# Kernel tuning notes

Hardware: AMD Instinct MI355X
Metric: run time of the kernel (lower is better)

The kernel has to match this reference:

```python
import jax, jax.numpy as jnp
import numpy as np

D_MODEL = 1024
NUM_HEADS = 16
D_K = D_MODEL // NUM_HEADS


def setup_inputs() -> dict:
    key = jax.random.key(0)
    ks = jax.random.split(key, 9)
    s = 1.0 / np.sqrt(D_MODEL)
    inp = {
        "x": jax.random.normal(ks[0], (4, 2048, D_MODEL), dtype=jnp.float32),
        "W_q": jax.random.uniform(ks[1], (D_MODEL, D_MODEL), jnp.float32, -s, s),
        "b_q": jax.random.uniform(ks[2], (D_MODEL,), jnp.float32, -s, s),
        "W_k": jax.random.uniform(ks[3], (D_MODEL, D_MODEL), jnp.float32, -s, s),
        "b_k": jax.random.uniform(ks[4], (D_MODEL,), jnp.float32, -s, s),
        "W_v": jax.random.uniform(ks[5], (D_MODEL, D_MODEL), jnp.float32, -s, s),
        "b_v": jax.random.uniform(ks[6], (D_MODEL,), jnp.float32, -s, s),
        "W_o": jax.random.uniform(ks[7], (D_MODEL, D_MODEL), jnp.float32, -s, s),
        "b_o": jax.random.uniform(ks[8], (D_MODEL,), jnp.float32, -s, s),
    }
    return inp


def reference(x, W_q, b_q, W_k, b_k, W_v, b_v, W_o, b_o):
    B, S, _ = x.shape
    # Linear layers (torch convention: y = x @ W.T + b), split into heads -> [B, H, S, d_k]
    def proj(W, b):
        y = jnp.einsum("bsd,ed->bse", x, W) + b
        return y.reshape(B, S, NUM_HEADS, D_K).transpose(0, 2, 1, 3)

    Q = proj(W_q, b_q)
    K = proj(W_k, b_k)
    V = proj(W_v, b_v)

    scale = 1.0 / jnp.sqrt(jnp.asarray(D_K, dtype=x.dtype))
    scores = jnp.einsum("bhqd,bhkd->bhqk", Q, K) * scale  # [B, H, S, S]
    attn = jax.nn.softmax(scores, axis=-1)
    out = jnp.einsum("bhqk,bhkd->bhqd", attn, V)  # [B, H, S, d_k]
    out = out.transpose(0, 2, 1, 3).reshape(B, S, D_MODEL)
    return jnp.einsum("bsd,ed->bse", out, W_o) + b_o
```

## Files before the change

### kernel.cpp

```cpp
#include <hip/hip_runtime.h>
#include <hip/hip_bf16.h>
#include <math.h>


constexpr int D = 1024;
constexpr int H = 16;
constexpr int DK = 64;
constexpr int PSTR = 72;

typedef unsigned short u16;
typedef __attribute__((ext_vector_type(8))) short v8s;
typedef __attribute__((ext_vector_type(4))) float v4f;
typedef const __attribute__((address_space(1))) void gvoid;
typedef __attribute__((address_space(3))) void lvoid;
typedef __attribute__((address_space(3))) u16 ls_u16;
typedef __attribute__((address_space(3))) v8s lv8s;

__device__ __forceinline__ u16 rne_bf16(float f) {
  unsigned u = __float_as_uint(f);
  u += 0x7FFFu + ((u >> 16) & 1u);
  return (u16)(u >> 16);
}

__device__ __forceinline__ unsigned pk_bf16(float a, float b) {
  __hip_bfloat162 t = __float22bfloat162_rn(float2{a, b});
  return *reinterpret_cast<unsigned*>(&t);
}

__device__ __forceinline__ void cfence() { asm volatile("" ::: "memory"); }

__device__ __forceinline__ void split_body(const float* __restrict__ in,
                                           u16* __restrict__ hi, u16* __restrict__ lo,
                                           int i)
{
  const float4 v = ((const float4*)in)[i];
  const float f[4] = {v.x, v.y, v.z, v.w};
  ushort4 h, l;
  u16 hh[4], ll[4];
#pragma unroll
  for (int j = 0; j < 4; ++j) {
    const unsigned u = __float_as_uint(f[j]);
    hh[j] = (u16)(u >> 16);
    const float hf = __uint_as_float(u & 0xFFFF0000u);
    ll[j] = rne_bf16(f[j] - hf);
  }
  h.x = hh[0]; h.y = hh[1]; h.z = hh[2]; h.w = hh[3];
  l.x = ll[0]; l.y = ll[1]; l.z = ll[2]; l.w = ll[3];
  ((ushort4*)hi)[i] = h;
  ((ushort4*)lo)[i] = l;
}

__global__ __launch_bounds__(256) void split_all_kernel(
    const float* __restrict__ x,
    const float* __restrict__ w0, const float* __restrict__ w1,
    const float* __restrict__ w2, const float* __restrict__ w3,
    u16* __restrict__ xs_hi, u16* __restrict__ xs_lo,
    u16* __restrict__ qkv_hi, u16* __restrict__ qkv_lo,
    u16* __restrict__ o_hi, u16* __restrict__ o_lo, int n4x)
{
  constexpr int N4W = (int)(D * (size_t)D / 4);
  const int i = blockIdx.x * 256 + threadIdx.x;
  if (i < n4x) {
    split_body(x, xs_hi, xs_lo, i);
    return;
  }
  const int t = i - n4x;
  const int y = t / N4W;
  const int j = t - y * N4W;
  if (y >= 4) return;
  const float* src = (y == 0) ? w0 : (y == 1) ? w1 : (y == 2) ? w2 : w3;
  const size_t off = (size_t)y * (size_t)(D * (size_t)D);
  u16* hi = (y < 3) ? qkv_hi + off : o_hi;
  u16* lo = (y < 3) ? qkv_lo + off : o_lo;
  split_body(src, hi, lo, j);
}

template<int R>
__device__ __forceinline__ void stage_arr(const u16* __restrict__ src, ls_u16* dst,
                                          int tid, int row0, int k0)
{
  const int cg = (tid & 3) ^ ((tid >> 3) & 3);
#pragma unroll
  for (int j = 0; j < R / 128; ++j) {
    const int row = j * 128 + (tid >> 2);
    __builtin_amdgcn_global_load_lds(
        (gvoid*)(src + (size_t)(row0 + row) * D + k0 + cg * 8),
        (lvoid*)(dst + j * 4096 + tid * 8), 16, 0, 0);
  }
}

template<int EPI>
__global__ __launch_bounds__(512, 2) void gemm_pipe_kernel(
    const u16* __restrict__ Ahi, const u16* __restrict__ Alo,
    const u16* __restrict__ Whi, const u16* __restrict__ Wlo,
    const float* __restrict__ b0v, const float* __restrict__ b1v, const float* __restrict__ b2v,
    u16* __restrict__ Qb, u16* __restrict__ Kb, u16* __restrict__ Vtb,
    float* __restrict__ C, int S_)
{
  constexpr int BM = 256, BN = 256;
  constexpr int TA = BM * 32;
  constexpr int TB = BN * 32;
  constexpr int BUFSZ = 2 * TA + 2 * TB;
  __shared__ u16 lds[2][BUFSZ];

  const int tid = threadIdx.x;
  const int lane = tid & 63, w = tid >> 6;
  const int wm = (w >> 2) * 128, wn = (w & 3) * 64;
  const int fr = lane & 15, fq = lane >> 4;
  const int csw = (fq ^ ((fr >> 1) & 3)) * 8;

  const int gx = gridDim.x;
  const int gyd = gridDim.y;
  const int nwg = gx * gyd;
  int id = blockIdx.y * gx + blockIdx.x;
  id = (id & 7) * (nwg >> 3) + (id >> 3);
  constexpr int GM = 4;
  const int per_grp = GM * gyd;
  const int grp = id / per_grp;
  const int ing = id - grp * per_grp;
  const int m0 = (grp * GM + (ing & (GM - 1))) * BM;
  const int n0 = (ing / GM) * BN;

  v4f acc[8][4];
#pragma unroll
  for (int mi = 0; mi < 8; ++mi)
#pragma unroll
    for (int ni = 0; ni < 4; ++ni) acc[mi][ni] = (v4f){0.f, 0.f, 0.f, 0.f};

  ls_u16* pb0 = (ls_u16*)&lds[0][0];
  ls_u16* pb1 = (ls_u16*)&lds[1][0];

  int aoff[8], boff[4];
#pragma unroll
  for (int i = 0; i < 8; ++i) aoff[i] = (wm + i * 16 + fr) * 32 + csw;
#pragma unroll
  for (int i = 0; i < 4; ++i) boff[i] = 2 * TA + (wn + i * 16 + fr) * 32 + csw;

  stage_arr<BM>(Ahi, pb0, tid, m0, 0);
  stage_arr<BM>(Alo, pb0 + TA, tid, m0, 0);
  stage_arr<BN>(Whi, pb0 + 2 * TA, tid, n0, 0);
  stage_arr<BN>(Wlo, pb0 + 2 * TA + TB, tid, n0, 0);
  asm volatile("s_waitcnt vmcnt(0)" ::: "memory");
  __builtin_amdgcn_s_barrier();
  cfence();

#pragma unroll 2
  for (int k = 0; k < 32; ++k) {
    const int ks = (k + 1 < 32) ? (k + 1) * 32 : 31 * 32;

    v8s ah[8], bh[4], tf[8];
#pragma unroll
    for (int i = 0; i < 8; ++i) ah[i] = *(const lv8s*)(pb0 + aoff[i]);
#pragma unroll
    for (int i = 0; i < 4; ++i) bh[i] = *(const lv8s*)(pb0 + boff[i]);
    stage_arr<BM>(Ahi, pb1, tid, m0, ks);
    stage_arr<BM>(Alo, pb1 + TA, tid, m0, ks);
    __builtin_amdgcn_s_setprio(1);
#pragma unroll
    for (int mi = 0; mi < 8; ++mi)
#pragma unroll
      for (int ni = 0; ni < 4; ++ni)
        acc[mi][ni] = __builtin_amdgcn_mfma_f32_16x16x32_bf16(ah[mi], bh[ni], acc[mi][ni], 0, 0, 0);
    __builtin_amdgcn_s_setprio(0);
    cfence();
    __builtin_amdgcn_s_barrier();
    cfence();

#pragma unroll
    for (int i = 0; i < 8; ++i) tf[i] = *(const lv8s*)(pb0 + TA + aoff[i]);
    stage_arr<BN>(Whi, pb1 + 2 * TA, tid, n0, ks);
    stage_arr<BN>(Wlo, pb1 + 2 * TA + TB, tid, n0, ks);
    __builtin_amdgcn_s_setprio(1);
#pragma unroll
    for (int mi = 0; mi < 8; ++mi)
#pragma unroll
      for (int ni = 0; ni < 4; ++ni)
        acc[mi][ni] = __builtin_amdgcn_mfma_f32_16x16x32_bf16(tf[mi], bh[ni], acc[mi][ni], 0, 0, 0);
    __builtin_amdgcn_s_setprio(0);
    cfence();
    __builtin_amdgcn_s_barrier();
    cfence();

#pragma unroll
    for (int i = 0; i < 4; ++i) tf[i] = *(const lv8s*)(pb0 + boff[i] + TB);
    __builtin_amdgcn_s_setprio(1);
#pragma unroll
    for (int mi = 0; mi < 8; ++mi)
#pragma unroll
      for (int ni = 0; ni < 4; ++ni)
        acc[mi][ni] = __builtin_amdgcn_mfma_f32_16x16x32_bf16(ah[mi], tf[ni], acc[mi][ni], 0, 0, 0);
    __builtin_amdgcn_s_setprio(0);
    cfence();

    asm volatile("s_waitcnt vmcnt(0)" ::: "memory");
    __builtin_amdgcn_s_barrier();
    cfence();

    ls_u16* t = pb0; pb0 = pb1; pb1 = t;
  }

  const int lane4 = fq * 4;
  if constexpr (EPI == 0) {
    const int wsel = n0 >> 10;
    const float* bias = (wsel == 0) ? b0v : (wsel == 1) ? b1v : b2v;
    u16* Cb = (wsel == 0) ? Qb : (wsel == 1) ? Kb : Vtb;
    const int bb = m0 / S_;
    const int s0 = m0 - bb * S_;
#pragma unroll
    for (int mi = 0; mi < 8; ++mi) {
#pragma unroll
      for (int ni = 0; ni < 4; ++ni) {
        const int n = n0 + wn + ni * 16 + fr;
        const int nl = n & (D - 1);
        const float bvv = bias[nl];
        const int h = nl >> 6, dk = nl & 63;
#pragma unroll
        for (int r = 0; r < 4; ++r) {
          const int s = s0 + wm + mi * 16 + lane4 + r;
          const float val = acc[mi][ni][r] + bvv;
          if (wsel < 2)
            Cb[((size_t)(bb * H + h) * S_ + s) * DK + dk] = rne_bf16(val);
          else
            Cb[((size_t)(bb * H + h) * DK + dk) * S_ + s] = rne_bf16(val);
        }
      }
    }
  } else {
#pragma unroll
    for (int mi = 0; mi < 8; ++mi)
#pragma unroll
      for (int ni = 0; ni < 4; ++ni) {
        const int n = n0 + wn + ni * 16 + fr;
        const float bvv = b0v[n];
#pragma unroll
        for (int r = 0; r < 4; ++r) {
          const int m = m0 + wm + mi * 16 + lane4 + r;
          C[(size_t)m * D + n] = acc[mi][ni][r] + bvv;
        }
      }
  }
}

__global__ __launch_bounds__(512, 4) void attn_mfma_kernel(
    const u16* __restrict__ Qb, const u16* __restrict__ Kb, const u16* __restrict__ Vtb,
    u16* __restrict__ Ohi, u16* __restrict__ Olo, int S_)
{
  __shared__ u16 Ks[2][64 * 64];
  __shared__ u16 Vt[2][64 * 64];
  __shared__ u16 Pl[8][32 * PSTR];

  const int tid = threadIdx.x;
  const int lane = tid & 63, w = tid >> 6;
  const int fr = lane & 15, fq = lane >> 4;

  const int gqx = gridDim.x;
  const int nwg = gqx * gridDim.y * gridDim.z;
  int id = (blockIdx.z * gridDim.y + blockIdx.y) * gqx + blockIdx.x;
  id = (id & 7) * (nwg >> 3) + (id >> 3);
  const int qx = id % gqx;
  const int rest = id / gqx;
  const int h = rest % H;
  const int b = rest / H;

  const int q0 = qx * 256;
  const int wq = w * 32;
  const size_t base = (size_t)(b * H + h) * S_ * DK;

  const int srow = tid >> 3;
  const int scb = (tid & 7) ^ (srow & 7);

  auto stage_kv = [&](int j0, int bufi) {
    __builtin_amdgcn_global_load_lds((gvoid*)(Kb + base + (size_t)(j0 + srow) * DK + scb * 8),
                                     (lvoid*)(&Ks[bufi][0] + tid * 8), 16, 0, 0);
    __builtin_amdgcn_global_load_lds((gvoid*)(Vtb + base + (size_t)srow * S_ + j0 + scb * 8),
                                     (lvoid*)(&Vt[bufi][0] + tid * 8), 16, 0, 0);
  };

  stage_kv(0, 0);

  v8s qa[2][2];
#pragma unroll
  for (int ni = 0; ni < 2; ++ni)
#pragma unroll
    for (int ks = 0; ks < 2; ++ks)
      qa[ni][ks] = *(const v8s*)(Qb + base + (size_t)(q0 + wq + ni * 16 + fr) * DK + ks * 32 + fq * 8);

  v4f o[4][2];
  float lsum[2] = {0.f, 0.f};
#pragma unroll
  for (int mi = 0; mi < 4; ++mi)
#pragma unroll
    for (int ni = 0; ni < 2; ++ni) o[mi][ni] = (v4f){0.f, 0.f, 0.f, 0.f};

  asm volatile("s_waitcnt vmcnt(0)" ::: "memory");
  __builtin_amdgcn_s_barrier();
  cfence();

  const int NT = S_ >> 6;
  for (int jt = 0; jt < NT; ++jt) {
    const int cur = jt & 1;
    if (jt + 1 < NT) stage_kv((jt + 1) * 64, cur ^ 1);

    const u16* Kc = &Ks[cur][0];
    const u16* Vc = &Vt[cur][0];

    v4f s[4][2];
#pragma unroll
    for (int mi = 0; mi < 4; ++mi)
#pragma unroll
      for (int ni = 0; ni < 2; ++ni) s[mi][ni] = (v4f){0.f, 0.f, 0.f, 0.f};
#pragma unroll
    for (int ks = 0; ks < 2; ++ks) {
      v8s kb[4];
#pragma unroll
      for (int mi = 0; mi < 4; ++mi) {
        const int row = mi * 16 + fr;
        kb[mi] = *(const v8s*)&Kc[row * 64 + (((ks * 4 + fq) ^ (row & 7)) * 8)];
      }
#pragma unroll
      for (int mi = 0; mi < 4; ++mi)
#pragma unroll
        for (int ni = 0; ni < 2; ++ni)
          s[mi][ni] = __builtin_amdgcn_mfma_f32_16x16x32_bf16(kb[mi], qa[ni][ks], s[mi][ni], 0, 0, 0);
    }

#pragma unroll
    for (int mi = 0; mi < 4; ++mi)
#pragma unroll
      for (int ni = 0; ni < 2; ++ni) {
        float p[4];
#pragma unroll
        for (int r = 0; r < 4; ++r) p[r] = __expf(s[mi][ni][r] * 0.125f);
        lsum[ni] += (p[0] + p[1]) + (p[2] + p[3]);
        uint2 pk;
        pk.x = pk_bf16(p[0], p[1]);
        pk.y = pk_bf16(p[2], p[3]);
        *(uint2*)&Pl[w][(ni * 16 + fr) * PSTR + mi * 16 + fq * 4] = pk;
      }

#pragma unroll
    for (int ks = 0; ks < 2; ++ks) {
      v8s vb[4], pa[2];
#pragma unroll
      for (int mi = 0; mi < 4; ++mi) {
        const int row = mi * 16 + fr;
        vb[mi] = *(const v8s*)&Vc[row * 64 + (((ks * 4 + fq) ^ (row & 7)) * 8)];
      }
#pragma unroll
      for (int ni = 0; ni < 2; ++ni)
        pa[ni] = *(const v8s*)&Pl[w][(ni * 16 + fr) * PSTR + ks * 32 + fq * 8];
#pragma unroll
      for (int mi = 0; mi < 4; ++mi)
#pragma unroll
        for (int ni = 0; ni < 2; ++ni)
          o[mi][ni] = __builtin_amdgcn_mfma_f32_16x16x32_bf16(vb[mi], pa[ni], o[mi][ni], 0, 0, 0);
    }

    asm volatile("s_waitcnt vmcnt(0)" ::: "memory");
    cfence();
    __builtin_amdgcn_s_barrier();
    cfence();
  }

  float linv[2];
#pragma unroll
  for (int ni = 0; ni < 2; ++ni) {
    float l = lsum[ni];
    l += __shfl_xor(l, 16);
    l += __shfl_xor(l, 32);
    linv[ni] = 1.f / l;
  }

#pragma unroll
  for (int ni = 0; ni < 2; ++ni) {
    const int q = q0 + wq + ni * 16 + fr;
    const size_t rowbase = (size_t)(b * S_ + q) * D + h * DK;
#pragma unroll
    for (int mi = 0; mi < 4; ++mi) {
      const int d0 = mi * 16 + fq * 4;
      float v[4];
      unsigned u[4];
      float res[4];
#pragma unroll
      for (int r = 0; r < 4; ++r) {
        v[r] = o[mi][ni][r] * linv[ni];
        u[r] = __float_as_uint(v[r]);
        res[r] = v[r] - __uint_as_float(u[r] & 0xFFFF0000u);
      }
      uint2 hi, lo;
      hi.x = (u[1] & 0xFFFF0000u) | (u[0] >> 16);
      hi.y = (u[3] & 0xFFFF0000u) | (u[2] >> 16);
      lo.x = pk_bf16(res[0], res[1]);
      lo.y = pk_bf16(res[2], res[3]);
      *(uint2*)(Ohi + rowbase + d0) = hi;
      *(uint2*)(Olo + rowbase + d0) = lo;
    }
  }
}

extern "C" void kernel_launch(void* const* d_in, const int* in_sizes, int n_in,
                              void* d_out, int out_size, void* d_ws, size_t ws_size,
                              hipStream_t stream) {
  const float* x  = (const float*)d_in[0];
  const float* Wq = (const float*)d_in[1];
  const float* bq = (const float*)d_in[2];
  const float* Wk = (const float*)d_in[3];
  const float* bk = (const float*)d_in[4];
  const float* Wv = (const float*)d_in[5];
  const float* bv = (const float*)d_in[6];
  const float* Wo = (const float*)d_in[7];
  const float* bo = (const float*)d_in[8];

  const int M = in_sizes[0] / D;
  const int B = 4;
  const int S_ = M / B;
  const size_t MD = (size_t)M * D;
  const size_t DD = (size_t)D * D;

  u16* Qb    = (u16*)d_ws;
  u16* Kb    = Qb + MD;
  u16* Vtb   = Kb + MD;
  u16* xs_hi = Vtb + MD;
  u16* xs_lo = xs_hi + MD;
  u16* Ohi   = xs_lo + MD;
  u16* Olo   = Ohi + MD;
  u16* wo_hi = Olo + MD;
  u16* wo_lo = wo_hi + DD;

  u16* wqkv_hi = (u16*)d_out;
  u16* wqkv_lo = wqkv_hi + 3 * DD;

  const int n4x = (int)(MD / 4);
  const int n4w = (int)(DD / 4);
  const int nsb = (n4x + 4 * n4w + 255) / 256;
  split_all_kernel<<<nsb, 256, 0, stream>>>(x, Wq, Wk, Wv, Wo,
                                            xs_hi, xs_lo, wqkv_hi, wqkv_lo,
                                            wo_hi, wo_lo, n4x);

  dim3 gq(M / 256, 3 * D / 256);
  gemm_pipe_kernel<0><<<gq, 512, 0, stream>>>(
      xs_hi, xs_lo, wqkv_hi, wqkv_lo, bq, bk, bv, Qb, Kb, Vtb, nullptr, S_);

  dim3 ga(S_ / 256, H, B);
  attn_mfma_kernel<<<ga, 512, 0, stream>>>(Qb, Kb, Vtb, Ohi, Olo, S_);

  dim3 go(M / 256, D / 256);
  gemm_pipe_kernel<1><<<go, 512, 0, stream>>>(
      Ohi, Olo, wo_hi, wo_lo, bo, nullptr, nullptr, nullptr, nullptr, nullptr,
      (float*)d_out, S_);
}
```

Baseline: 427.0 us.

## Shrink GEMM N-tiles, repartition waves, and use partial vmcnt waits in pipeline

Makes the GEMM N-tile a template parameter: 192 for the QKV projection and 128 for the output projection. This raises the workgroup count (QKV 32x16, out 32x8) so the grid fills more of the CUs. Waves are re-laid out as a 4x2 grid over 64-row slabs. The loop is reordered so that hi/lo W tiles are staged together and barriers wait on partial vmcnt counts instead of draining all loads, which lets the prefetch of the next K-slice overlap compute. It also drops the separate prologue barrier and moves the Q/K/V selection into the epilogue per column, since a 192-wide tile can straddle matrix boundaries. The risks are smaller per-wave MFMA blocks with lower operand reuse, and vmcnt counts that must exactly match how many loads were issued.

New measurement: 395.2 us. 1.08x faster.

```diff
diff --git a/kernel.cpp b/kernel.cpp
--- a/kernel.cpp
+++ b/kernel.cpp
@@ -89,7 +89,24 @@
   }
 }
 
-template<int EPI>
+template<int BN>
+__device__ __forceinline__ void stage_b(const u16* __restrict__ hi_src,
+                                        const u16* __restrict__ lo_src,
+                                        ls_u16* dst, int tid, int n0, int k0)
+{
+  const int cg = (tid & 3) ^ ((tid >> 3) & 3);
+#pragma unroll
+  for (int j = 0; j < (2 * BN) / 128; ++j) {
+    const int row = j * 128 + (tid >> 2);
+    const u16* s = (row < BN) ? hi_src : lo_src;
+    const int gr = (row < BN) ? row : row - BN;
+    __builtin_amdgcn_global_load_lds(
+        (gvoid*)(s + (size_t)(n0 + gr) * D + k0 + cg * 8),
+        (lvoid*)(dst + j * 4096 + tid * 8), 16, 0, 0);
+  }
+}
+
+template<int BN, int EPI>
 __global__ __launch_bounds__(512, 2) void gemm_pipe_kernel(
     const u16* __restrict__ Ahi, const u16* __restrict__ Alo,
     const u16* __restrict__ Whi, const u16* __restrict__ Wlo,
@@ -97,15 +114,18 @@
     u16* __restrict__ Qb, u16* __restrict__ Kb, u16* __restrict__ Vtb,
     float* __restrict__ C, int S_)
 {
-  constexpr int BM = 256, BN = 256;
+  constexpr int BM = 256;
   constexpr int TA = BM * 32;
   constexpr int TB = BN * 32;
   constexpr int BUFSZ = 2 * TA + 2 * TB;
+  constexpr int RM = 4;
+  constexpr int RN = BN / 32;
+  constexpr int XL = 2 + (2 * BN) / 128;
   __shared__ u16 lds[2][BUFSZ];
 
   const int tid = threadIdx.x;
   const int lane = tid & 63, w = tid >> 6;
-  const int wm = (w >> 2) * 128, wn = (w & 3) * 64;
+  const int wm = (w >> 1) * 64, wn = (w & 1) * (BN / 2);
   const int fr = lane & 15, fq = lane >> 4;
   const int csw = (fq ^ ((fr >> 1) & 3)) * 8;
 
@@ -121,79 +141,78 @@
   const int m0 = (grp * GM + (ing & (GM - 1))) * BM;
   const int n0 = (ing / GM) * BN;
 
-  v4f acc[8][4];
-#pragma unroll
-  for (int mi = 0; mi < 8; ++mi)
-#pragma unroll
-    for (int ni = 0; ni < 4; ++ni) acc[mi][ni] = (v4f){0.f, 0.f, 0.f, 0.f};
+  v4f acc[RM][RN];
+#pragma unroll
+  for (int mi = 0; mi < RM; ++mi)
+#pragma unroll
+    for (int ni = 0; ni < RN; ++ni) acc[mi][ni] = (v4f){0.f, 0.f, 0.f, 0.f};
 
   ls_u16* pb0 = (ls_u16*)&lds[0][0];
   ls_u16* pb1 = (ls_u16*)&lds[1][0];
 
-  int aoff[8], boff[4];
-#pragma unroll
-  for (int i = 0; i < 8; ++i) aoff[i] = (wm + i * 16 + fr) * 32 + csw;
-#pragma unroll
-  for (int i = 0; i < 4; ++i) boff[i] = 2 * TA + (wn + i * 16 + fr) * 32 + csw;
+  int aoff[RM], boff[RN];
+#pragma unroll
+  for (int i = 0; i < RM; ++i) aoff[i] = (wm + i * 16 + fr) * 32 + csw;
+#pragma unroll
+  for (int i = 0; i < RN; ++i) boff[i] = 2 * TA + (wn + i * 16 + fr) * 32 + csw;
 
   stage_arr<BM>(Ahi, pb0, tid, m0, 0);
+  stage_b<BN>(Whi, Wlo, pb0 + 2 * TA, tid, n0, 0);
   stage_arr<BM>(Alo, pb0 + TA, tid, m0, 0);
-  stage_arr<BN>(Whi, pb0 + 2 * TA, tid, n0, 0);
-  stage_arr<BN>(Wlo, pb0 + 2 * TA + TB, tid, n0, 0);
-  asm volatile("s_waitcnt vmcnt(0)" ::: "memory");
-  __builtin_amdgcn_s_barrier();
-  cfence();
 
 #pragma unroll 2
   for (int k = 0; k < 32; ++k) {
     const int ks = (k + 1 < 32) ? (k + 1) * 32 : 31 * 32;
 
-    v8s ah[8], bh[4], tf[8];
-#pragma unroll
-    for (int i = 0; i < 8; ++i) ah[i] = *(const lv8s*)(pb0 + aoff[i]);
-#pragma unroll
-    for (int i = 0; i < 4; ++i) bh[i] = *(const lv8s*)(pb0 + boff[i]);
+    asm volatile("s_waitcnt vmcnt(2)" ::: "memory");
+    __builtin_amdgcn_s_barrier();
+    cfence();
+    v8s ah[RM], bh[RN];
+#pragma unroll
+    for (int i = 0; i < RM; ++i) ah[i] = *(const lv8s*)(pb0 + aoff[i]);
+#pragma unroll
+    for (int i = 0; i < RN; ++i) bh[i] = *(const lv8s*)(pb0 + boff[i]);
     stage_arr<BM>(Ahi, pb1, tid, m0, ks);
+    stage_b<BN>(Whi, Wlo, pb1 + 2 * TA, tid, n0, ks);
+    __builtin_amdgcn_s_setprio(1);
+#pragma unroll
+    for (int mi = 0; mi < RM; ++mi)
+#pragma unroll
+      for (int ni = 0; ni < RN; ++ni)
+        acc[mi][ni] = __builtin_amdgcn_mfma_f32_16x16x32_bf16(ah[mi], bh[ni], acc[mi][ni], 0, 0, 0);
+    __builtin_amdgcn_s_setprio(0);
+    cfence();
+
+    if constexpr (XL == 5) {
+      asm volatile("s_waitcnt vmcnt(5)" ::: "memory");
+    } else {
+      asm volatile("s_waitcnt vmcnt(4)" ::: "memory");
+    }
+    __builtin_amdgcn_s_barrier();
+    cfence();
+    v8s ta[RM];
+#pragma unroll
+    for (int i = 0; i < RM; ++i) ta[i] = *(const lv8s*)(pb0 + TA + aoff[i]);
     stage_arr<BM>(Alo, pb1 + TA, tid, m0, ks);
     __builtin_amdgcn_s_setprio(1);
 #pragma unroll
-    for (int mi = 0; mi < 8; ++mi)
-#pragma unroll
-      for (int ni = 0; ni < 4; ++ni)
-        acc[mi][ni] = __builtin_amdgcn_mfma_f32_16x16x32_bf16(ah[mi], bh[ni], acc[mi][ni], 0, 0, 0);
+    for (int mi = 0; mi < RM; ++mi)
+#pragma unroll
+      for (int ni = 0; ni < RN; ++ni)
+        acc[mi][ni] = __builtin_amdgcn_mfma_f32_16x16x32_bf16(ta[mi], bh[ni], acc[mi][ni], 0, 0, 0);
     __builtin_amdgcn_s_setprio(0);
     cfence();
-    __builtin_amdgcn_s_barrier();
-    cfence();
-
-#pragma unroll
-    for (int i = 0; i < 8; ++i) tf[i] = *(const lv8s*)(pb0 + TA + aoff[i]);
-    stage_arr<BN>(Whi, pb1 + 2 * TA, tid, n0, ks);
-    stage_arr<BN>(Wlo, pb1 + 2 * TA + TB, tid, n0, ks);
+
+    v8s tb[RN];
+#pragma unroll
+    for (int i = 0; i < RN; ++i) tb[i] = *(const lv8s*)(pb0 + boff[i] + TB);
     __builtin_amdgcn_s_setprio(1);
 #pragma unroll
-    for (int mi = 0; mi < 8; ++mi)
-#pragma unroll
-      for (int ni = 0; ni < 4; ++ni)
-        acc[mi][ni] = __builtin_amdgcn_mfma_f32_16x16x32_bf16(tf[mi], bh[ni], acc[mi][ni], 0, 0, 0);
+    for (int mi = 0; mi < RM; ++mi)
+#pragma unroll
+      for (int ni = 0; ni < RN; ++ni)
+        acc[mi][ni] = __builtin_amdgcn_mfma_f32_16x16x32_bf16(ah[mi], tb[ni], acc[mi][ni], 0, 0, 0);
     __builtin_amdgcn_s_setprio(0);
-    cfence();
-    __builtin_amdgcn_s_barrier();
-    cfence();
-
-#pragma unroll
-    for (int i = 0; i < 4; ++i) tf[i] = *(const lv8s*)(pb0 + boff[i] + TB);
-    __builtin_amdgcn_s_setprio(1);
-#pragma unroll
-    for (int mi = 0; mi < 8; ++mi)
-#pragma unroll
-      for (int ni = 0; ni < 4; ++ni)
-        acc[mi][ni] = __builtin_amdgcn_mfma_f32_16x16x32_bf16(ah[mi], tf[ni], acc[mi][ni], 0, 0, 0);
-    __builtin_amdgcn_s_setprio(0);
-    cfence();
-
-    asm volatile("s_waitcnt vmcnt(0)" ::: "memory");
-    __builtin_amdgcn_s_barrier();
     cfence();
 
     ls_u16* t = pb0; pb0 = pb1; pb1 = t;
@@ -201,16 +220,16 @@
 
   const int lane4 = fq * 4;
   if constexpr (EPI == 0) {
-    const int wsel = n0 >> 10;
-    const float* bias = (wsel == 0) ? b0v : (wsel == 1) ? b1v : b2v;
-    u16* Cb = (wsel == 0) ? Qb : (wsel == 1) ? Kb : Vtb;
     const int bb = m0 / S_;
     const int s0 = m0 - bb * S_;
 #pragma unroll
-    for (int mi = 0; mi < 8; ++mi) {
-#pragma unroll
-      for (int ni = 0; ni < 4; ++ni) {
+    for (int mi = 0; mi < RM; ++mi) {
+#pragma unroll
+      for (int ni = 0; ni < RN; ++ni) {
         const int n = n0 + wn + ni * 16 + fr;
+        const int wsel = n >> 10;
+        const float* bias = (wsel == 0) ? b0v : (wsel == 1) ? b1v : b2v;
+        u16* Cb = (wsel == 0) ? Qb : (wsel == 1) ? Kb : Vtb;
         const int nl = n & (D - 1);
         const float bvv = bias[nl];
         const int h = nl >> 6, dk = nl & 63;
@@ -227,9 +246,9 @@
     }
   } else {
 #pragma unroll
-    for (int mi = 0; mi < 8; ++mi)
-#pragma unroll
-      for (int ni = 0; ni < 4; ++ni) {
+    for (int mi = 0; mi < RM; ++mi)
+#pragma unroll
+      for (int ni = 0; ni < RN; ++ni) {
         const int n = n0 + wn + ni * 16 + fr;
         const float bvv = b0v[n];
 #pragma unroll
@@ -437,15 +456,15 @@
                                             xs_hi, xs_lo, wqkv_hi, wqkv_lo,
                                             wo_hi, wo_lo, n4x);
 
-  dim3 gq(M / 256, 3 * D / 256);
-  gemm_pipe_kernel<0><<<gq, 512, 0, stream>>>(
+  dim3 gq(M / 256, 3 * D / 192);
+  gemm_pipe_kernel<192, 0><<<gq, 512, 0, stream>>>(
       xs_hi, xs_lo, wqkv_hi, wqkv_lo, bq, bk, bv, Qb, Kb, Vtb, nullptr, S_);
 
   dim3 ga(S_ / 256, H, B);
   attn_mfma_kernel<<<ga, 512, 0, stream>>>(Qb, Kb, Vtb, Ohi, Olo, S_);
 
-  dim3 go(M / 256, D / 256);
-  gemm_pipe_kernel<1><<<go, 512, 0, stream>>>(
+  dim3 go(M / 256, D / 128);
+  gemm_pipe_kernel<128, 1><<<go, 512, 0, stream>>>(
       Ohi, Olo, wo_hi, wo_lo, bo, nullptr, nullptr, nullptr, nullptr, nullptr,
       (float*)d_out, S_);
 }
```
